# Performance work log

Hardware: AMD Instinct MI355X
Metric: run time of the kernel (lower is better)

The kernel has to match this reference:

```python
import jax, jax.numpy as jnp
import numpy as np

BATCH = 2048
DIM = 256
HID = 512
NCLS = 10
TPTS = 8
SUBSTEPS = 4  # fixed dopri5 substeps per time interval


def setup_inputs() -> dict:
    key = jax.random.key(0)
    ks = jax.random.split(key, 8)
    s1 = 1.0 / np.sqrt(DIM)
    s2 = 1.0 / np.sqrt(HID)
    return {
        "x0": jax.random.normal(ks[0], (BATCH, DIM), jnp.float32),
        "t": jnp.arange(TPTS, dtype=jnp.float32) / (TPTS - 1),
        "W1": jax.random.normal(ks[1], (DIM, HID), jnp.float32) * s1,
        "b1": jnp.zeros((HID,), jnp.float32),
        "W2": jax.random.normal(ks[2], (HID, DIM), jnp.float32) * s2,
        "b2": jnp.zeros((DIM,), jnp.float32),
        "Wc1": jax.random.normal(ks[3], (DIM, 64), jnp.float32) * s1,
        "bc1": jnp.zeros((64,), jnp.float32),
        "Wc2": jax.random.normal(ks[4], (64, NCLS), jnp.float32) * 0.125,
        "bc2": jnp.zeros((NCLS,), jnp.float32),
    }


def reference(x0, t, W1, b1, W2, b2, Wc1, bc1, Wc2, bc2):
    # ODE function: dy/dt = f(t, y) = tanh(y @ W1 + b1) @ W2 + b2
    def f(ti, y):
        return jnp.tanh(y @ W1 + b1) @ W2 + b2

    # Fixed substep grid: SUBSTEPS equal dopri5 steps per [t_i, t_{i+1}] interval.
    dt_int = (t[1:] - t[:-1]) / SUBSTEPS                      # [TPTS-1]
    frac = jnp.arange(SUBSTEPS, dtype=t.dtype)
    starts = (t[:-1, None] + dt_int[:, None] * frac).reshape(-1)  # [(TPTS-1)*SUBSTEPS]
    dts = jnp.repeat(dt_int, SUBSTEPS)

    def dopri5_step(y, td):
        ti, dt = td
        k1 = f(ti, y)
        k2 = f(ti + dt * (1.0 / 5), y + dt * (1.0 / 5) * k1)
        k3 = f(ti + dt * (3.0 / 10), y + dt * (3.0 / 40 * k1 + 9.0 / 40 * k2))
        k4 = f(ti + dt * (4.0 / 5), y + dt * (44.0 / 45 * k1 - 56.0 / 15 * k2 + 32.0 / 9 * k3))
        k5 = f(ti + dt * (8.0 / 9), y + dt * (19372.0 / 6561 * k1 - 25360.0 / 2187 * k2
                                              + 64448.0 / 6561 * k3 - 212.0 / 729 * k4))
        k6 = f(ti + dt, y + dt * (9017.0 / 3168 * k1 - 355.0 / 33 * k2 + 46732.0 / 5247 * k3
                                  + 49.0 / 176 * k4 - 5103.0 / 18656 * k5))
        # 5th-order solution weights (b7 = 0, FSAL)
        y_next = y + dt * (35.0 / 384 * k1 + 500.0 / 1113 * k3 + 125.0 / 192 * k4
                           - 2187.0 / 6784 * k5 + 11.0 / 84 * k6)
        return y_next, None

    yT, _ = jax.lax.scan(dopri5_step, x0, (starts, dts))  # final state at t[-1]

    # classifier head (Dropout is identity in eval mode)
    h = jax.nn.relu(yT @ Wc1 + bc1)
    logits = h @ Wc2 + bc2
    return logits
```

## Files before the change

### kernel.cpp

```cpp
#include <hip/hip_runtime.h>

typedef _Float16 f16;
typedef _Float16 f16x2 __attribute__((ext_vector_type(2)));
typedef _Float16 f16x8 __attribute__((ext_vector_type(8)));
typedef float f32x4 __attribute__((ext_vector_type(4)));

#define DIM 256
#define HID 512

#define WSO_W1  0
#define WSO_W2  131072
#define WSO_WC1 262144
#define WSO_WC2 278528
#define PACK_TOTAL 279552

#define LDS_W1   0
#define LDS_YST  131072
#define LDS_HB   139264
#define SMEM_BYTES 155648

#define MFMA(a, b, c) __builtin_amdgcn_mfma_f32_16x16x32_f16(a, b, c, 0, 0, 0)

__global__ void pack_weights(const float* __restrict__ W1, const float* __restrict__ W2,
                             const float* __restrict__ Wc1, const float* __restrict__ Wc2,
                             f16* __restrict__ ws) {
    int gid = blockIdx.x * 256 + threadIdx.x;
    if (gid >= PACK_TOTAL) return;
    if (gid < WSO_W2) {
        int g = gid;
        int j = g & 7, lane = (g >> 3) & 63, fi = g >> 9;
        int kt = fi >> 5, nt = fi & 31;
        int k = kt * 32 + ((lane >> 4) << 3) + j;
        int n = (nt << 4) + (lane & 15);
        ws[WSO_W1 + g] = (f16)W1[k * HID + n];
    } else if (gid < WSO_WC1) {
        int g = gid - WSO_W2;
        int j = g & 7, lane = (g >> 3) & 63, fi = g >> 9;
        int kt = fi >> 4, nt = fi & 15;
        int k = kt * 32 + ((lane >> 4) << 3) + j;
        int n = (nt << 4) + (lane & 15);
        ws[WSO_W2 + g] = (f16)W2[k * DIM + n];
    } else if (gid < WSO_WC2) {
        int g = gid - WSO_WC1;
        int j = g & 7, lane = (g >> 3) & 63, fi = g >> 9;
        int kt = fi >> 2, nt = fi & 3;
        int k = kt * 32 + ((lane >> 4) << 3) + j;
        int n = (nt << 4) + (lane & 15);
        ws[WSO_WC1 + g] = (f16)Wc1[k * 64 + n];
    } else {
        int g = gid - WSO_WC2;
        int j = g & 7, lane = (g >> 3) & 63, kt = g >> 9;
        int k = kt * 32 + ((lane >> 4) << 3) + j;
        int n = lane & 15;
        ws[WSO_WC2 + g] = (n < 10) ? (f16)Wc2[k * 10 + n] : (f16)0.0f;
    }
}

__device__ __forceinline__ float tanh_fast(float x) {
    float e = __expf(2.0f * x);
    return 1.0f - 2.0f * __builtin_amdgcn_rcpf(e + 1.0f);
}

template <class FIN, class FOUT>
__device__ __forceinline__ void feval(FIN yin, FOUT kout,
        const f16* __restrict__ ws, const f16* w1lds, f16* yst, f16* hbuf,
        int lane, int w, const float b1c[4], const float b2c[2]) {
    const int cn   = lane & 15;
    const int rlo  = (lane >> 4) << 2;
    const int koff = (lane >> 4) << 3;

#define LDW1(KT, Q) (*(const f16x8*)(ws + WSO_W1 + ((((KT) * 32 + 4 * w + (Q)) << 9) + lane * 8)))
#define LDW2(KT, T) (*(const f16x8*)(ws + WSO_W2 + ((((KT) * 16 + 2 * w + (T)) << 9) + lane * 8)))

    #pragma unroll
    for (int t = 0; t < 2; ++t)
        #pragma unroll
        for (int i = 0; i < 4; ++i) {
            int row = rlo + i;
            int col = w * 32 + t * 16 + cn;
            int idx = ((row << 8) + col) ^ ((row & 7) << 3);
            yst[idx] = (f16)yin(t, i);
        }
    __syncthreads();

    f16x8 w1s[4];
    #pragma unroll
    for (int q = 0; q < 4; ++q) w1s[q] = LDW1(0, q);

    f32x4 acc[4];
    #pragma unroll
    for (int q = 0; q < 4; ++q) acc[q] = (f32x4){0.f, 0.f, 0.f, 0.f};

#define M1_LDS(KT) { \
        int aidx = ((cn << 8) + (KT) * 32 + koff) ^ ((cn & 7) << 3); \
        f16x8 af = *(const f16x8*)(yst + aidx); \
        _Pragma("unroll") \
        for (int q = 0; q < 4; ++q) { \
            f16x8 wf = *(const f16x8*)(w1lds + ((((KT) - 4) * 32 + 4 * w + q) << 9) + lane * 8); \
            acc[q] = MFMA(af, wf, acc[q]); } }
#define M1_STR(KT, RKT, DOREF) { \
        int aidx = ((cn << 8) + (KT) * 32 + koff) ^ ((cn & 7) << 3); \
        f16x8 af = *(const f16x8*)(yst + aidx); \
        f16x8 t0 = w1s[0], t1 = w1s[1], t2 = w1s[2], t3 = w1s[3]; \
        if (DOREF) { \
            w1s[0] = LDW1(RKT, 0); w1s[1] = LDW1(RKT, 1); \
            w1s[2] = LDW1(RKT, 2); w1s[3] = LDW1(RKT, 3); } \
        acc[0] = MFMA(af, t0, acc[0]); acc[1] = MFMA(af, t1, acc[1]); \
        acc[2] = MFMA(af, t2, acc[2]); acc[3] = MFMA(af, t3, acc[3]); }

    M1_LDS(4)
    M1_LDS(5)
    M1_STR(0, 1, 1)
    M1_LDS(6)
    M1_STR(1, 2, 1)
    M1_LDS(7)
    M1_STR(2, 3, 1)
    M1_STR(3, 3, 0)
#undef M1_LDS
#undef M1_STR

    #pragma unroll
    for (int q = 0; q < 4; ++q) {
        int hcol = ((4 * w + q) << 4) + cn;
        #pragma unroll
        for (int i = 0; i < 4; ++i) {
            float th = tanh_fast(acc[q][i] + b1c[q]);
            int row = rlo + i;
            int idx = ((row << 9) + hcol) ^ ((row & 7) << 3);
            hbuf[idx] = (f16)th;
        }
    }
    __syncthreads();

    f16x8 w2s[4][2];
    #pragma unroll
    for (int st = 0; st < 4; ++st) {
        w2s[st][0] = LDW2(st, 0);
        w2s[st][1] = LDW2(st, 1);
    }

    f32x4 acc2[2];
    acc2[0] = (f32x4){0.f, 0.f, 0.f, 0.f};
    acc2[1] = (f32x4){0.f, 0.f, 0.f, 0.f};

#define M2(KT) { \
        int aidx = ((cn << 9) + (KT) * 32 + koff) ^ ((cn & 7) << 3); \
        f16x8 af = *(const f16x8*)(hbuf + aidx); \
        f16x8 b0 = w2s[(KT) & 3][0], b1v = w2s[(KT) & 3][1]; \
        if ((KT) < 12) { \
            w2s[(KT) & 3][0] = LDW2((KT) + 4, 0); \
            w2s[(KT) & 3][1] = LDW2((KT) + 4, 1); } \
        acc2[0] = MFMA(af, b0, acc2[0]); \
        acc2[1] = MFMA(af, b1v, acc2[1]); }

    M2(0)  M2(1)  M2(2)  M2(3)
    M2(4)  M2(5)  M2(6)  M2(7)
    M2(8)  M2(9)  M2(10) M2(11)
    M2(12) M2(13) M2(14) M2(15)
#undef M2
#undef LDW1
#undef LDW2

    #pragma unroll
    for (int t = 0; t < 2; ++t)
        #pragma unroll
        for (int i = 0; i < 4; ++i)
            kout(t, i, acc2[t][i] + b2c[t]);
}

__launch_bounds__(512)
__global__ void ode_main(const float* __restrict__ x0, const float* __restrict__ tg,
                         const float* __restrict__ b1, const float* __restrict__ b2,
                         const float* __restrict__ bc1, const float* __restrict__ bc2,
                         const f16* __restrict__ ws, float* __restrict__ out) {
    extern __shared__ char smem[];
    f16* w1lds = (f16*)(smem + LDS_W1);
    f16* yst   = (f16*)(smem + LDS_YST);
    f16* hbuf  = (f16*)(smem + LDS_HB);

    const int tid  = threadIdx.x;
    const int lane = tid & 63;
    const int w    = tid >> 6;
    const int r0   = blockIdx.x * 16;
    const int cn   = lane & 15;
    const int rlo  = (lane >> 4) << 2;

    #pragma unroll
    for (int u = 0; u < 16; ++u) {
        int e = (u * 512 + tid) * 8;
        *(f16x8*)(w1lds + e) = *(const f16x8*)(ws + WSO_W1 + 65536 + e);
    }

    float b1c[4], b2c[2];
    #pragma unroll
    for (int q = 0; q < 4; ++q) b1c[q] = b1[((4 * w + q) << 4) + cn];
    #pragma unroll
    for (int t = 0; t < 2; ++t) b2c[t] = b2[((2 * w + t) << 4) + cn];

    float y[2][4];
    #pragma unroll
    for (int t = 0; t < 2; ++t)
        #pragma unroll
        for (int i = 0; i < 4; ++i)
            y[t][i] = x0[(r0 + rlo + i) * DIM + w * 32 + t * 16 + cn];

    __syncthreads();

    f16x2 k1p[2][2], k2p[2][2], k3p[2][2], k4p[2][2], k5p[2][2];
    float dt = 0.f;

#define KGET(P, t, i) ((float)P[t][(i) >> 1][(i) & 1])
#define KPUT(P, t, i, v) P[t][(i) >> 1][(i) & 1] = (f16)(v)

    for (int s = 0; s < 28; ++s) {
        if ((s & 3) == 0) { int iv = s >> 2; dt = (tg[iv + 1] - tg[iv]) * 0.25f; }

        feval([&](int t, int i) { return y[t][i]; },
              [&](int t, int i, float v) { KPUT(k1p, t, i, v); },
              ws, w1lds, yst, hbuf, lane, w, b1c, b2c);
        feval([&](int t, int i) { return y[t][i] + dt * 0.2f * KGET(k1p, t, i); },
              [&](int t, int i, float v) { KPUT(k2p, t, i, v); },
              ws, w1lds, yst, hbuf, lane, w, b1c, b2c);
        feval([&](int t, int i) { return y[t][i] + dt * (0.075f * KGET(k1p, t, i) + 0.225f * KGET(k2p, t, i)); },
              [&](int t, int i, float v) { KPUT(k3p, t, i, v); },
              ws, w1lds, yst, hbuf, lane, w, b1c, b2c);
        feval([&](int t, int i) { return y[t][i] + dt * ((44.f/45.f) * KGET(k1p, t, i) + (-56.f/15.f) * KGET(k2p, t, i)
                                                        + (32.f/9.f) * KGET(k3p, t, i)); },
              [&](int t, int i, float v) { KPUT(k4p, t, i, v); },
              ws, w1lds, yst, hbuf, lane, w, b1c, b2c);
        feval([&](int t, int i) { return y[t][i] + dt * ((19372.f/6561.f) * KGET(k1p, t, i) + (-25360.f/2187.f) * KGET(k2p, t, i)
                                                        + (64448.f/6561.f) * KGET(k3p, t, i) + (-212.f/729.f) * KGET(k4p, t, i)); },
              [&](int t, int i, float v) { KPUT(k5p, t, i, v); },
              ws, w1lds, yst, hbuf, lane, w, b1c, b2c);
        feval([&](int t, int i) { return y[t][i] + dt * ((9017.f/3168.f) * KGET(k1p, t, i) + (-355.f/33.f) * KGET(k2p, t, i)
                                                        + (46732.f/5247.f) * KGET(k3p, t, i) + (49.f/176.f) * KGET(k4p, t, i)
                                                        + (-5103.f/18656.f) * KGET(k5p, t, i)); },
              [&](int t, int i, float v) {
                  y[t][i] += dt * ((35.f/384.f)    * KGET(k1p, t, i) + (500.f/1113.f)  * KGET(k3p, t, i)
                                 + (125.f/192.f)   * KGET(k4p, t, i) + (-2187.f/6784.f) * KGET(k5p, t, i)
                                 + (11.f/84.f)     * v);
              },
              ws, w1lds, yst, hbuf, lane, w, b1c, b2c);
    }
#undef KGET
#undef KPUT

    #pragma unroll
    for (int t = 0; t < 2; ++t)
        #pragma unroll
        for (int i = 0; i < 4; ++i) {
            int row = rlo + i;
            int col = w * 32 + t * 16 + cn;
            int idx = ((row << 8) + col) ^ ((row & 7) << 3);
            yst[idx] = (f16)y[t][i];
        }
    __syncthreads();

    if (w < 4) {
        const int koff = (lane >> 4) << 3;
        f32x4 ha = (f32x4){0.f, 0.f, 0.f, 0.f};
        #pragma unroll
        for (int kt = 0; kt < 8; ++kt) {
            int aidx = ((cn << 8) + kt * 32 + koff) ^ ((cn & 7) << 3);
            f16x8 af = *(const f16x8*)(yst + aidx);
            f16x8 wf = *(const f16x8*)(ws + WSO_WC1 + (((kt * 4 + w) << 9) + lane * 8));
            ha = MFMA(af, wf, ha);
        }
        float bb = bc1[(w << 4) + cn];
        #pragma unroll
        for (int i = 0; i < 4; ++i) {
            float v = fmaxf(ha[i] + bb, 0.f);
            int row = rlo + i;
            int idx = ((row << 6) + (w << 4) + cn) ^ ((row & 7) << 3);
            hbuf[idx] = (f16)v;
        }
    }
    __syncthreads();

    if (w == 0) {
        const int koff = (lane >> 4) << 3;
        f32x4 acc = (f32x4){0.f, 0.f, 0.f, 0.f};
        #pragma unroll
        for (int kt = 0; kt < 2; ++kt) {
            int aidx = ((cn << 6) + kt * 32 + koff) ^ ((cn & 7) << 3);
            f16x8 af = *(const f16x8*)(hbuf + aidx);
            f16x8 wf = *(const f16x8*)(ws + WSO_WC2 + ((kt << 9) + lane * 8));
            acc = MFMA(af, wf, acc);
        }
        if (cn < 10) {
            float bb = bc2[cn];
            #pragma unroll
            for (int i = 0; i < 4; ++i)
                out[(r0 + rlo + i) * 10 + cn] = acc[i] + bb;
        }
    }
}

extern "C" void kernel_launch(void* const* d_in, const int* in_sizes, int n_in,
                              void* d_out, int out_size, void* d_ws, size_t ws_size,
                              hipStream_t stream) {
    const float* x0  = (const float*)d_in[0];
    const float* tg  = (const float*)d_in[1];
    const float* W1  = (const float*)d_in[2];
    const float* b1  = (const float*)d_in[3];
    const float* W2  = (const float*)d_in[4];
    const float* b2  = (const float*)d_in[5];
    const float* Wc1 = (const float*)d_in[6];
    const float* bc1 = (const float*)d_in[7];
    const float* Wc2 = (const float*)d_in[8];
    const float* bc2 = (const float*)d_in[9];
    f16* ws = (f16*)d_ws;
    float* out = (float*)d_out;

    hipFuncSetAttribute((const void*)ode_main,
                        hipFuncAttributeMaxDynamicSharedMemorySize, SMEM_BYTES);

    pack_weights<<<(PACK_TOTAL + 255) / 256, 256, 0, stream>>>(W1, W2, Wc1, Wc2, ws);
    ode_main<<<128, 512, SMEM_BYTES, stream>>>(x0, tg, b1, b2, bc1, bc2, ws, out);
}
```

Before: 1.630 ms.

## Spill RK stages to LDS and stream more W1 tiles from global

Moves the k1-k4 stage values out of registers into a per-thread LDS region, and shrinks the LDS-resident W1 slice from four k-tiles to three. The first two k-tiles are now held in two alternating register windows, streamed from global, to make room for the stage buffer. The aim is to cut VGPR pressure and the prefetch stalls in the first GEMM. In exchange it adds LDS traffic on every stage combination and more global W1 reads per evaluation.

```diff
diff --git a/kernel.cpp b/kernel.cpp
--- a/kernel.cpp
+++ b/kernel.cpp
@@ -15,8 +15,9 @@
 #define PACK_TOTAL 279552
 
 #define LDS_W1   0
-#define LDS_YST  131072
-#define LDS_HB   139264
+#define LDS_YST  98304
+#define LDS_HB   106496
+#define LDS_K    122880
 #define SMEM_BYTES 155648
 
 #define MFMA(a, b, c) __builtin_amdgcn_mfma_f32_16x16x32_f16(a, b, c, 0, 0, 0)
@@ -83,9 +84,11 @@
         }
     __syncthreads();
 
-    f16x8 w1s[4];
-    #pragma unroll
-    for (int q = 0; q < 4; ++q) w1s[q] = LDW1(0, q);
+    f16x8 wA[4], wB[4];
+    #pragma unroll
+    for (int q = 0; q < 4; ++q) wA[q] = LDW1(0, q);
+    #pragma unroll
+    for (int q = 0; q < 4; ++q) wB[q] = LDW1(1, q);
 
     f32x4 acc[4];
     #pragma unroll
@@ -96,26 +99,26 @@
         f16x8 af = *(const f16x8*)(yst + aidx); \
         _Pragma("unroll") \
         for (int q = 0; q < 4; ++q) { \
-            f16x8 wf = *(const f16x8*)(w1lds + ((((KT) - 4) * 32 + 4 * w + q) << 9) + lane * 8); \
+            f16x8 wf = *(const f16x8*)(w1lds + ((((KT) - 5) * 32 + 4 * w + q) << 9) + lane * 8); \
             acc[q] = MFMA(af, wf, acc[q]); } }
-#define M1_STR(KT, RKT, DOREF) { \
+#define M1_STR(KT, WIN, RKT, DOREF) { \
         int aidx = ((cn << 8) + (KT) * 32 + koff) ^ ((cn & 7) << 3); \
         f16x8 af = *(const f16x8*)(yst + aidx); \
-        f16x8 t0 = w1s[0], t1 = w1s[1], t2 = w1s[2], t3 = w1s[3]; \
+        f16x8 t0 = WIN[0], t1 = WIN[1], t2 = WIN[2], t3 = WIN[3]; \
         if (DOREF) { \
-            w1s[0] = LDW1(RKT, 0); w1s[1] = LDW1(RKT, 1); \
-            w1s[2] = LDW1(RKT, 2); w1s[3] = LDW1(RKT, 3); } \
+            WIN[0] = LDW1(RKT, 0); WIN[1] = LDW1(RKT, 1); \
+            WIN[2] = LDW1(RKT, 2); WIN[3] = LDW1(RKT, 3); } \
         acc[0] = MFMA(af, t0, acc[0]); acc[1] = MFMA(af, t1, acc[1]); \
         acc[2] = MFMA(af, t2, acc[2]); acc[3] = MFMA(af, t3, acc[3]); }
 
-    M1_LDS(4)
     M1_LDS(5)
-    M1_STR(0, 1, 1)
     M1_LDS(6)
-    M1_STR(1, 2, 1)
+    M1_STR(0, wA, 2, 1)
     M1_LDS(7)
-    M1_STR(2, 3, 1)
-    M1_STR(3, 3, 0)
+    M1_STR(1, wB, 3, 1)
+    M1_STR(2, wA, 4, 1)
+    M1_STR(3, wB, 0, 0)
+    M1_STR(4, wA, 0, 0)
 #undef M1_LDS
 #undef M1_STR
 
@@ -162,10 +165,12 @@
 #undef LDW2
 
     #pragma unroll
-    for (int t = 0; t < 2; ++t)
-        #pragma unroll
-        for (int i = 0; i < 4; ++i)
-            kout(t, i, acc2[t][i] + b2c[t]);
+    for (int t = 0; t < 2; ++t) {
+        f32x4 v = acc2[t];
+        #pragma unroll
+        for (int i = 0; i < 4; ++i) v[i] += b2c[t];
+        kout(t, v);
+    }
 }
 
 __launch_bounds__(512)
@@ -177,6 +182,7 @@
     f16* w1lds = (f16*)(smem + LDS_W1);
     f16* yst   = (f16*)(smem + LDS_YST);
     f16* hbuf  = (f16*)(smem + LDS_HB);
+    f16* klds  = (f16*)(smem + LDS_K);
 
     const int tid  = threadIdx.x;
     const int lane = tid & 63;
@@ -186,9 +192,9 @@
     const int rlo  = (lane >> 4) << 2;
 
     #pragma unroll
-    for (int u = 0; u < 16; ++u) {
+    for (int u = 0; u < 12; ++u) {
         int e = (u * 512 + tid) * 8;
-        *(f16x8*)(w1lds + e) = *(const f16x8*)(ws + WSO_W1 + 65536 + e);
+        *(f16x8*)(w1lds + e) = *(const f16x8*)(ws + WSO_W1 + 81920 + e);
     }
 
     float b1c[4], b2c[2];
@@ -196,6 +202,17 @@
     for (int q = 0; q < 4; ++q) b1c[q] = b1[((4 * w + q) << 4) + cn];
     #pragma unroll
     for (int t = 0; t < 2; ++t) b2c[t] = b2[((2 * w + t) << 4) + cn];
+
+    auto kput = [&](int kid, int t, f32x4 v) {
+        f16x2 p0; p0[0] = (f16)v[0]; p0[1] = (f16)v[1];
+        f16x2 p1; p1[0] = (f16)v[2]; p1[1] = (f16)v[3];
+        *(f16x2*)(klds + (((kid << 2) + (t << 1) + 0) << 10) + tid * 2) = p0;
+        *(f16x2*)(klds + (((kid << 2) + (t << 1) + 1) << 10) + tid * 2) = p1;
+    };
+    auto kget = [&](int kid, int t, int i) -> float {
+        f16x2 p = *(const f16x2*)(klds + (((kid << 2) + (t << 1) + (i >> 1)) << 10) + tid * 2);
+        return (float)p[i & 1];
+    };
 
     float y[2][4];
     #pragma unroll
@@ -206,44 +223,47 @@
 
     __syncthreads();
 
-    f16x2 k1p[2][2], k2p[2][2], k3p[2][2], k4p[2][2], k5p[2][2];
+    f16x2 k5p[2][2];
     float dt = 0.f;
 
-#define KGET(P, t, i) ((float)P[t][(i) >> 1][(i) & 1])
-#define KPUT(P, t, i, v) P[t][(i) >> 1][(i) & 1] = (f16)(v)
+#define K5GET(t, i) ((float)k5p[t][(i) >> 1][(i) & 1])
 
     for (int s = 0; s < 28; ++s) {
         if ((s & 3) == 0) { int iv = s >> 2; dt = (tg[iv + 1] - tg[iv]) * 0.25f; }
 
         feval([&](int t, int i) { return y[t][i]; },
-              [&](int t, int i, float v) { KPUT(k1p, t, i, v); },
-              ws, w1lds, yst, hbuf, lane, w, b1c, b2c);
-        feval([&](int t, int i) { return y[t][i] + dt * 0.2f * KGET(k1p, t, i); },
-              [&](int t, int i, float v) { KPUT(k2p, t, i, v); },
-              ws, w1lds, yst, hbuf, lane, w, b1c, b2c);
-        feval([&](int t, int i) { return y[t][i] + dt * (0.075f * KGET(k1p, t, i) + 0.225f * KGET(k2p, t, i)); },
-              [&](int t, int i, float v) { KPUT(k3p, t, i, v); },
-              ws, w1lds, yst, hbuf, lane, w, b1c, b2c);
-        feval([&](int t, int i) { return y[t][i] + dt * ((44.f/45.f) * KGET(k1p, t, i) + (-56.f/15.f) * KGET(k2p, t, i)
-                                                        + (32.f/9.f) * KGET(k3p, t, i)); },
-              [&](int t, int i, float v) { KPUT(k4p, t, i, v); },
-              ws, w1lds, yst, hbuf, lane, w, b1c, b2c);
-        feval([&](int t, int i) { return y[t][i] + dt * ((19372.f/6561.f) * KGET(k1p, t, i) + (-25360.f/2187.f) * KGET(k2p, t, i)
-                                                        + (64448.f/6561.f) * KGET(k3p, t, i) + (-212.f/729.f) * KGET(k4p, t, i)); },
-              [&](int t, int i, float v) { KPUT(k5p, t, i, v); },
-              ws, w1lds, yst, hbuf, lane, w, b1c, b2c);
-        feval([&](int t, int i) { return y[t][i] + dt * ((9017.f/3168.f) * KGET(k1p, t, i) + (-355.f/33.f) * KGET(k2p, t, i)
-                                                        + (46732.f/5247.f) * KGET(k3p, t, i) + (49.f/176.f) * KGET(k4p, t, i)
-                                                        + (-5103.f/18656.f) * KGET(k5p, t, i)); },
-              [&](int t, int i, float v) {
-                  y[t][i] += dt * ((35.f/384.f)    * KGET(k1p, t, i) + (500.f/1113.f)  * KGET(k3p, t, i)
-                                 + (125.f/192.f)   * KGET(k4p, t, i) + (-2187.f/6784.f) * KGET(k5p, t, i)
-                                 + (11.f/84.f)     * v);
+              [&](int t, f32x4 v) { kput(0, t, v); },
+              ws, w1lds, yst, hbuf, lane, w, b1c, b2c);
+        feval([&](int t, int i) { return y[t][i] + dt * 0.2f * kget(0, t, i); },
+              [&](int t, f32x4 v) { kput(1, t, v); },
+              ws, w1lds, yst, hbuf, lane, w, b1c, b2c);
+        feval([&](int t, int i) { return y[t][i] + dt * (0.075f * kget(0, t, i) + 0.225f * kget(1, t, i)); },
+              [&](int t, f32x4 v) { kput(2, t, v); },
+              ws, w1lds, yst, hbuf, lane, w, b1c, b2c);
+        feval([&](int t, int i) { return y[t][i] + dt * ((44.f/45.f) * kget(0, t, i) + (-56.f/15.f) * kget(1, t, i)
+                                                        + (32.f/9.f) * kget(2, t, i)); },
+              [&](int t, f32x4 v) { kput(3, t, v); },
+              ws, w1lds, yst, hbuf, lane, w, b1c, b2c);
+        feval([&](int t, int i) { return y[t][i] + dt * ((19372.f/6561.f) * kget(0, t, i) + (-25360.f/2187.f) * kget(1, t, i)
+                                                        + (64448.f/6561.f) * kget(2, t, i) + (-212.f/729.f) * kget(3, t, i)); },
+              [&](int t, f32x4 v) {
+                  k5p[t][0][0] = (f16)v[0]; k5p[t][0][1] = (f16)v[1];
+                  k5p[t][1][0] = (f16)v[2]; k5p[t][1][1] = (f16)v[3];
               },
               ws, w1lds, yst, hbuf, lane, w, b1c, b2c);
-    }
-#undef KGET
-#undef KPUT
+        feval([&](int t, int i) { return y[t][i] + dt * ((9017.f/3168.f) * kget(0, t, i) + (-355.f/33.f) * kget(1, t, i)
+                                                        + (46732.f/5247.f) * kget(2, t, i) + (49.f/176.f) * kget(3, t, i)
+                                                        + (-5103.f/18656.f) * K5GET(t, i)); },
+              [&](int t, f32x4 v) {
+                  #pragma unroll
+                  for (int i = 0; i < 4; ++i)
+                      y[t][i] += dt * ((35.f/384.f)    * kget(0, t, i) + (500.f/1113.f)  * kget(2, t, i)
+                                     + (125.f/192.f)   * kget(3, t, i) + (-2187.f/6784.f) * K5GET(t, i)
+                                     + (11.f/84.f)     * v[i]);
+              },
+              ws, w1lds, yst, hbuf, lane, w, b1c, b2c);
+    }
+#undef K5GET
 
     #pragma unroll
     for (int t = 0; t < 2; ++t)
```

After: 1.680 ms. 1.03x slower.

## Halve waves per block and keep part of W2 resident in registers

Applied to the files above, without the earlier changes.

The ODE kernel now uses 256 threads (4 waves) per block instead of 512, so each wave covers twice as many output columns in both GEMMs. The first 6 k-tiles of W2 stay in registers for the whole integration, and the remaining W2 tiles are streamed from global memory. The goal is fewer global/L2 weight reads per f-evaluation and less barrier cost per wave. The trade-off is much higher register pressure and fewer waves available to hide latency, which is forced with waves_per_eu(1,1).

```diff
diff --git a/kernel.cpp b/kernel.cpp
--- a/kernel.cpp
+++ b/kernel.cpp
@@ -64,111 +64,140 @@
 template <class FIN, class FOUT>
 __device__ __forceinline__ void feval(FIN yin, FOUT kout,
         const f16* __restrict__ ws, const f16* w1lds, f16* yst, f16* hbuf,
-        int lane, int w, const float b1c[4], const float b2c[2]) {
+        const f16x8 (&w2r)[4][6],
+        int lane, int w, const float b1c[8], const float b2c[4]) {
     const int cn   = lane & 15;
     const int rlo  = (lane >> 4) << 2;
     const int koff = (lane >> 4) << 3;
 
-#define LDW1(KT, Q) (*(const f16x8*)(ws + WSO_W1 + ((((KT) * 32 + 4 * w + (Q)) << 9) + lane * 8)))
-#define LDW2(KT, T) (*(const f16x8*)(ws + WSO_W2 + ((((KT) * 16 + 2 * w + (T)) << 9) + lane * 8)))
-
-    #pragma unroll
-    for (int t = 0; t < 2; ++t)
+#define LDW1F(KT, NT) (*(const f16x8*)(ws + WSO_W1 + ((((KT) * 32 + (NT)) << 9) + lane * 8)))
+#define LDW2F(KT, NT) (*(const f16x8*)(ws + WSO_W2 + ((((KT) * 16 + (NT)) << 9) + lane * 8)))
+
+    #pragma unroll
+    for (int t = 0; t < 4; ++t)
         #pragma unroll
         for (int i = 0; i < 4; ++i) {
             int row = rlo + i;
-            int col = w * 32 + t * 16 + cn;
+            int col = (w << 6) + (t << 4) + cn;
             int idx = ((row << 8) + col) ^ ((row & 7) << 3);
             yst[idx] = (f16)yin(t, i);
         }
     __syncthreads();
 
-    f16x8 w1s[4];
-    #pragma unroll
-    for (int q = 0; q < 4; ++q) w1s[q] = LDW1(0, q);
-
-    f32x4 acc[4];
-    #pragma unroll
-    for (int q = 0; q < 4; ++q) acc[q] = (f32x4){0.f, 0.f, 0.f, 0.f};
-
-#define M1_LDS(KT) { \
+    #pragma unroll
+    for (int hh = 0; hh < 2; ++hh) {
+        const int nb = 8 * w + 4 * hh;
+        f16x8 wA[4], wB[4];
+        #pragma unroll
+        for (int q = 0; q < 4; ++q) wA[q] = LDW1F(0, nb + q);
+        #pragma unroll
+        for (int q = 0; q < 4; ++q) wB[q] = LDW1F(1, nb + q);
+
+        f32x4 acc[4];
+        #pragma unroll
+        for (int q = 0; q < 4; ++q) acc[q] = (f32x4){0.f, 0.f, 0.f, 0.f};
+
+#define M1L(KT) { \
         int aidx = ((cn << 8) + (KT) * 32 + koff) ^ ((cn & 7) << 3); \
         f16x8 af = *(const f16x8*)(yst + aidx); \
         _Pragma("unroll") \
         for (int q = 0; q < 4; ++q) { \
-            f16x8 wf = *(const f16x8*)(w1lds + ((((KT) - 4) * 32 + 4 * w + q) << 9) + lane * 8); \
+            f16x8 wf = *(const f16x8*)(w1lds + ((((KT) - 4) * 32 + nb + q) << 9) + lane * 8); \
             acc[q] = MFMA(af, wf, acc[q]); } }
-#define M1_STR(KT, RKT, DOREF) { \
+#define M1S(KT, WIN, RKT, DOREF) { \
         int aidx = ((cn << 8) + (KT) * 32 + koff) ^ ((cn & 7) << 3); \
         f16x8 af = *(const f16x8*)(yst + aidx); \
-        f16x8 t0 = w1s[0], t1 = w1s[1], t2 = w1s[2], t3 = w1s[3]; \
+        f16x8 t0 = WIN[0], t1 = WIN[1], t2 = WIN[2], t3 = WIN[3]; \
         if (DOREF) { \
-            w1s[0] = LDW1(RKT, 0); w1s[1] = LDW1(RKT, 1); \
-            w1s[2] = LDW1(RKT, 2); w1s[3] = LDW1(RKT, 3); } \
+            WIN[0] = LDW1F(RKT, nb + 0); WIN[1] = LDW1F(RKT, nb + 1); \
+            WIN[2] = LDW1F(RKT, nb + 2); WIN[3] = LDW1F(RKT, nb + 3); } \
         acc[0] = MFMA(af, t0, acc[0]); acc[1] = MFMA(af, t1, acc[1]); \
         acc[2] = MFMA(af, t2, acc[2]); acc[3] = MFMA(af, t3, acc[3]); }
 
-    M1_LDS(4)
-    M1_LDS(5)
-    M1_STR(0, 1, 1)
-    M1_LDS(6)
-    M1_STR(1, 2, 1)
-    M1_LDS(7)
-    M1_STR(2, 3, 1)
-    M1_STR(3, 3, 0)
-#undef M1_LDS
-#undef M1_STR
-
-    #pragma unroll
-    for (int q = 0; q < 4; ++q) {
-        int hcol = ((4 * w + q) << 4) + cn;
-        #pragma unroll
-        for (int i = 0; i < 4; ++i) {
-            float th = tanh_fast(acc[q][i] + b1c[q]);
-            int row = rlo + i;
-            int idx = ((row << 9) + hcol) ^ ((row & 7) << 3);
-            hbuf[idx] = (f16)th;
-        }
-    }
-    __syncthreads();
-
-    f16x8 w2s[4][2];
-    #pragma unroll
-    for (int st = 0; st < 4; ++st) {
-        w2s[st][0] = LDW2(st, 0);
-        w2s[st][1] = LDW2(st, 1);
-    }
-
-    f32x4 acc2[2];
-    acc2[0] = (f32x4){0.f, 0.f, 0.f, 0.f};
-    acc2[1] = (f32x4){0.f, 0.f, 0.f, 0.f};
-
-#define M2(KT) { \
+        M1L(4)
+        M1L(5)
+        M1S(0, wA, 2, 1)
+        M1L(6)
+        M1S(1, wB, 3, 1)
+        M1L(7)
+        M1S(2, wA, 0, 0)
+        M1S(3, wB, 0, 0)
+#undef M1L
+#undef M1S
+
+        #pragma unroll
+        for (int q = 0; q < 4; ++q) {
+            int hcol = ((nb + q) << 4) + cn;
+            #pragma unroll
+            for (int i = 0; i < 4; ++i) {
+                float th = tanh_fast(acc[q][i] + b1c[4 * hh + q]);
+                int row = rlo + i;
+                int idx = ((row << 9) + hcol) ^ ((row & 7) << 3);
+                hbuf[idx] = (f16)th;
+            }
+        }
+    }
+    __syncthreads();
+
+    f16x8 w2s[2][4];
+    #pragma unroll
+    for (int t = 0; t < 4; ++t) w2s[0][t] = LDW2F(6, 4 * w + t);
+    #pragma unroll
+    for (int t = 0; t < 4; ++t) w2s[1][t] = LDW2F(7, 4 * w + t);
+
+    f32x4 acc2[4];
+    #pragma unroll
+    for (int t = 0; t < 4; ++t) acc2[t] = (f32x4){0.f, 0.f, 0.f, 0.f};
+
+#define M2R(KT) { \
         int aidx = ((cn << 9) + (KT) * 32 + koff) ^ ((cn & 7) << 3); \
         f16x8 af = *(const f16x8*)(hbuf + aidx); \
-        f16x8 b0 = w2s[(KT) & 3][0], b1v = w2s[(KT) & 3][1]; \
-        if ((KT) < 12) { \
-            w2s[(KT) & 3][0] = LDW2((KT) + 4, 0); \
-            w2s[(KT) & 3][1] = LDW2((KT) + 4, 1); } \
-        acc2[0] = MFMA(af, b0, acc2[0]); \
-        acc2[1] = MFMA(af, b1v, acc2[1]); }
-
-    M2(0)  M2(1)  M2(2)  M2(3)
-    M2(4)  M2(5)  M2(6)  M2(7)
-    M2(8)  M2(9)  M2(10) M2(11)
-    M2(12) M2(13) M2(14) M2(15)
-#undef M2
-#undef LDW1
-#undef LDW2
-
-    #pragma unroll
-    for (int t = 0; t < 2; ++t)
-        #pragma unroll
-        for (int i = 0; i < 4; ++i)
-            kout(t, i, acc2[t][i] + b2c[t]);
-}
-
-__launch_bounds__(512)
+        acc2[0] = MFMA(af, w2r[0][KT], acc2[0]); \
+        acc2[1] = MFMA(af, w2r[1][KT], acc2[1]); \
+        acc2[2] = MFMA(af, w2r[2][KT], acc2[2]); \
+        acc2[3] = MFMA(af, w2r[3][KT], acc2[3]); }
+#define M2S(KT, SL, RKT, DOREF) { \
+        int aidx = ((cn << 9) + (KT) * 32 + koff) ^ ((cn & 7) << 3); \
+        f16x8 af = *(const f16x8*)(hbuf + aidx); \
+        f16x8 t0 = w2s[SL][0], t1 = w2s[SL][1], t2 = w2s[SL][2], t3 = w2s[SL][3]; \
+        if (DOREF) { \
+            w2s[SL][0] = LDW2F(RKT, 4 * w + 0); w2s[SL][1] = LDW2F(RKT, 4 * w + 1); \
+            w2s[SL][2] = LDW2F(RKT, 4 * w + 2); w2s[SL][3] = LDW2F(RKT, 4 * w + 3); } \
+        acc2[0] = MFMA(af, t0, acc2[0]); acc2[1] = MFMA(af, t1, acc2[1]); \
+        acc2[2] = MFMA(af, t2, acc2[2]); acc2[3] = MFMA(af, t3, acc2[3]); }
+
+    M2S(6, 0, 8, 1)
+    M2S(7, 1, 9, 1)
+    M2R(0)
+    M2R(1)
+    M2S(8, 0, 10, 1)
+    M2S(9, 1, 11, 1)
+    M2R(2)
+    M2R(3)
+    M2S(10, 0, 12, 1)
+    M2S(11, 1, 13, 1)
+    M2R(4)
+    M2R(5)
+    M2S(12, 0, 14, 1)
+    M2S(13, 1, 15, 1)
+    M2S(14, 0, 0, 0)
+    M2S(15, 1, 0, 0)
+#undef M2R
+#undef M2S
+#undef LDW1F
+#undef LDW2F
+
+    #pragma unroll
+    for (int t = 0; t < 4; ++t) {
+        f32x4 v = acc2[t];
+        #pragma unroll
+        for (int i = 0; i < 4; ++i) v[i] += b2c[t];
+        kout(t, v);
+    }
+}
+
+__launch_bounds__(256, 1)
+__attribute__((amdgpu_waves_per_eu(1, 1)))
 __global__ void ode_main(const float* __restrict__ x0, const float* __restrict__ tg,
                          const float* __restrict__ b1, const float* __restrict__ b2,
                          const float* __restrict__ bc1, const float* __restrict__ bc2,
@@ -186,77 +215,87 @@
     const int rlo  = (lane >> 4) << 2;
 
     #pragma unroll
-    for (int u = 0; u < 16; ++u) {
-        int e = (u * 512 + tid) * 8;
+    for (int u = 0; u < 32; ++u) {
+        int e = (u * 256 + tid) * 8;
         *(f16x8*)(w1lds + e) = *(const f16x8*)(ws + WSO_W1 + 65536 + e);
     }
 
-    float b1c[4], b2c[2];
-    #pragma unroll
-    for (int q = 0; q < 4; ++q) b1c[q] = b1[((4 * w + q) << 4) + cn];
-    #pragma unroll
-    for (int t = 0; t < 2; ++t) b2c[t] = b2[((2 * w + t) << 4) + cn];
-
-    float y[2][4];
-    #pragma unroll
-    for (int t = 0; t < 2; ++t)
+    f16x8 w2r[4][6];
+    #pragma unroll
+    for (int t = 0; t < 4; ++t)
+        #pragma unroll
+        for (int kt = 0; kt < 6; ++kt)
+            w2r[t][kt] = *(const f16x8*)(ws + WSO_W2 + (((kt * 16 + 4 * w + t) << 9) + lane * 8));
+
+    float b1c[8], b2c[4];
+    #pragma unroll
+    for (int q = 0; q < 8; ++q) b1c[q] = b1[((8 * w + q) << 4) + cn];
+    #pragma unroll
+    for (int t = 0; t < 4; ++t) b2c[t] = b2[((4 * w + t) << 4) + cn];
+
+    float y[4][4];
+    #pragma unroll
+    for (int t = 0; t < 4; ++t)
         #pragma unroll
         for (int i = 0; i < 4; ++i)
-            y[t][i] = x0[(r0 + rlo + i) * DIM + w * 32 + t * 16 + cn];
-
-    __syncthreads();
-
-    f16x2 k1p[2][2], k2p[2][2], k3p[2][2], k4p[2][2], k5p[2][2];
+            y[t][i] = x0[(r0 + rlo + i) * DIM + (w << 6) + (t << 4) + cn];
+
+    __syncthreads();
+
+    f16x2 k1p[4][2], k2p[4][2], k3p[4][2], k4p[4][2], k5p[4][2];
     float dt = 0.f;
 
 #define KGET(P, t, i) ((float)P[t][(i) >> 1][(i) & 1])
-#define KPUT(P, t, i, v) P[t][(i) >> 1][(i) & 1] = (f16)(v)
+#define KPUTV(P, t, v) { P[t][0][0] = (f16)v[0]; P[t][0][1] = (f16)v[1]; \
+                         P[t][1][0] = (f16)v[2]; P[t][1][1] = (f16)v[3]; }
 
     for (int s = 0; s < 28; ++s) {
         if ((s & 3) == 0) { int iv = s >> 2; dt = (tg[iv + 1] - tg[iv]) * 0.25f; }
 
         feval([&](int t, int i) { return y[t][i]; },
-              [&](int t, int i, float v) { KPUT(k1p, t, i, v); },
-              ws, w1lds, yst, hbuf, lane, w, b1c, b2c);
+              [&](int t, f32x4 v) { KPUTV(k1p, t, v); },
+              ws, w1lds, yst, hbuf, w2r, lane, w, b1c, b2c);
         feval([&](int t, int i) { return y[t][i] + dt * 0.2f * KGET(k1p, t, i); },
-              [&](int t, int i, float v) { KPUT(k2p, t, i, v); },
-              ws, w1lds, yst, hbuf, lane, w, b1c, b2c);
+              [&](int t, f32x4 v) { KPUTV(k2p, t, v); },
+              ws, w1lds, yst, hbuf, w2r, lane, w, b1c, b2c);
         feval([&](int t, int i) { return y[t][i] + dt * (0.075f * KGET(k1p, t, i) + 0.225f * KGET(k2p, t, i)); },
-              [&](int t, int i, float v) { KPUT(k3p, t, i, v); },
-              ws, w1lds, yst, hbuf, lane, w, b1c, b2c);
+              [&](int t, f32x4 v) { KPUTV(k3p, t, v); },
+              ws, w1lds, yst, hbuf, w2r, lane, w, b1c, b2c);
         feval([&](int t, int i) { return y[t][i] + dt * ((44.f/45.f) * KGET(k1p, t, i) + (-56.f/15.f) * KGET(k2p, t, i)
                                                         + (32.f/9.f) * KGET(k3p, t, i)); },
-              [&](int t, int i, float v) { KPUT(k4p, t, i, v); },
-              ws, w1lds, yst, hbuf, lane, w, b1c, b2c);
+              [&](int t, f32x4 v) { KPUTV(k4p, t, v); },
+              ws, w1lds, yst, hbuf, w2r, lane, w, b1c, b2c);
         feval([&](int t, int i) { return y[t][i] + dt * ((19372.f/6561.f) * KGET(k1p, t, i) + (-25360.f/2187.f) * KGET(k2p, t, i)
                                                         + (64448.f/6561.f) * KGET(k3p, t, i) + (-212.f/729.f) * KGET(k4p, t, i)); },
-              [&](int t, int i, float v) { KPUT(k5p, t, i, v); },
-              ws, w1lds, yst, hbuf, lane, w, b1c, b2c);
+              [&](int t, f32x4 v) { KPUTV(k5p, t, v); },
+              ws, w1lds, yst, hbuf, w2r, lane, w, b1c, b2c);
         feval([&](int t, int i) { return y[t][i] + dt * ((9017.f/3168.f) * KGET(k1p, t, i) + (-355.f/33.f) * KGET(k2p, t, i)
                                                         + (46732.f/5247.f) * KGET(k3p, t, i) + (49.f/176.f) * KGET(k4p, t, i)
                                                         + (-5103.f/18656.f) * KGET(k5p, t, i)); },
-              [&](int t, int i, float v) {
-                  y[t][i] += dt * ((35.f/384.f)    * KGET(k1p, t, i) + (500.f/1113.f)  * KGET(k3p, t, i)
-                                 + (125.f/192.f)   * KGET(k4p, t, i) + (-2187.f/6784.f) * KGET(k5p, t, i)
-                                 + (11.f/84.f)     * v);
+              [&](int t, f32x4 v) {
+                  #pragma unroll
+                  for (int i = 0; i < 4; ++i)
+                      y[t][i] += dt * ((35.f/384.f)    * KGET(k1p, t, i) + (500.f/1113.f)  * KGET(k3p, t, i)
+                                     + (125.f/192.f)   * KGET(k4p, t, i) + (-2187.f/6784.f) * KGET(k5p, t, i)
+                                     + (11.f/84.f)     * v[i]);
               },
-              ws, w1lds, yst, hbuf, lane, w, b1c, b2c);
+              ws, w1lds, yst, hbuf, w2r, lane, w, b1c, b2c);
     }
 #undef KGET
-#undef KPUT
-
-    #pragma unroll
-    for (int t = 0; t < 2; ++t)
+#undef KPUTV
+
+    #pragma unroll
+    for (int t = 0; t < 4; ++t)
         #pragma unroll
         for (int i = 0; i < 4; ++i) {
             int row = rlo + i;
-            int col = w * 32 + t * 16 + cn;
+            int col = (w << 6) + (t << 4) + cn;
             int idx = ((row << 8) + col) ^ ((row & 7) << 3);
             yst[idx] = (f16)y[t][i];
         }
     __syncthreads();
 
-    if (w < 4) {
+    {
         const int koff = (lane >> 4) << 3;
         f32x4 ha = (f32x4){0.f, 0.f, 0.f, 0.f};
         #pragma unroll
@@ -316,5 +355,5 @@
                         hipFuncAttributeMaxDynamicSharedMemorySize, SMEM_BYTES);
 
     pack_weights<<<(PACK_TOTAL + 255) / 256, 256, 0, stream>>>(W1, W2, Wc1, Wc2, ws);
-    ode_main<<<128, 512, SMEM_BYTES, stream>>>(x0, tg, b1, b2, bc1, bc2, ws, out);
-}
+    ode_main<<<128, 256, SMEM_BYTES, stream>>>(x0, tg, b1, b2, bc1, bc2, ws, out);
+}
```

Measured after the change: 2.176 ms. +33.4%, slower.
